# Kernel tuning notes

Measured on AMD Instinct MI355X. Metric: run time of the kernel, lower is better.

The kernel has to match this reference:

```python
import jax, jax.numpy as jnp
import numpy as np

B, N, D, H = 4, 4096, 512, 8
K = D // H  # per-head dim = 64


def setup_inputs() -> dict:
    key = jax.random.key(0)
    k1, k2, k3, k4 = jax.random.split(key, 4)
    x = jax.random.normal(k1, (B, N, D), dtype=jnp.float32)
    # Conv1d(D, K, 1, bias=False) -> weight matrix [K, D], kaiming fan_out
    Wa = jax.random.normal(k2, (K, D), dtype=jnp.float32) * np.float32(np.sqrt(2.0 / K))
    # Conv1d(K, 1, 1) -> weight vector [K], bias scalar (init 0.01)
    Wb = jax.random.normal(k3, (K,), dtype=jnp.float32) * np.float32(np.sqrt(2.0))
    Wc = jax.random.normal(k4, (K,), dtype=jnp.float32) * np.float32(np.sqrt(2.0))
    wb_bias = jnp.full((), 0.01, dtype=jnp.float32)
    wc_bias = jnp.full((), 0.01, dtype=jnp.float32)
    bias = jnp.full((K,), 0.01, dtype=jnp.float32)
    return {"batchinput": x, "Wa": Wa, "Wb": Wb, "wb_bias": wb_bias,
            "Wc": Wc, "wc_bias": wc_bias, "bias": bias}


def reference(batchinput, Wa, Wb, wb_bias, Wc, wc_bias, bias):
    # single step (n_steps=1); all n_head heads share weights, so mean over
    # identical heads equals one head (dropout=0.0 -> identity).
    h = jnp.einsum('bnd,kd->bnk', batchinput, Wa)            # [B,N,K] projected feats
    t1 = jnp.einsum('bnk,k->bn', h, Wb) + wb_bias            # [B,N]
    t2 = jnp.einsum('bnk,k->bn', h, Wc) + wc_bias            # [B,N]
    scores = t1[:, :, None] + t2[:, None, :]                 # [B,N,N] additive score
    coefs = jax.nn.softmax(jax.nn.leaky_relu(scores, negative_slope=0.2), axis=-1)
    out = jnp.einsum('bnm,bmk->bnk', coefs, h) + bias        # [B,N,K]
    return out
```

## Files before the change

kernel.cpp:

```cpp
#include <hip/hip_runtime.h>
#include <hip/hip_bf16.h>

constexpr int cB = 4;
constexpr int cN = 4096;
constexpr int cD = 512;
constexpr int cK = 64;
constexpr int cNB = cB * cN;
constexpr int cNP = cN + 1;
constexpr int cCS = 16;
constexpr int cNC = cN / cCS;
constexpr int cNC1 = cNC + 1;

typedef unsigned short u16;
typedef unsigned int u32;
typedef unsigned long long u64;
typedef __bf16 bf16x8 __attribute__((ext_vector_type(8)));
typedef float f32x4 __attribute__((ext_vector_type(4)));

constexpr size_t OFF_H    = 0;
constexpr size_t OFF_T1   = OFF_H    + (size_t)cNB * cK;
constexpr size_t OFF_T2   = OFF_T1   + cNB;
constexpr size_t OFF_T2S  = OFF_T2   + cNB;
constexpr size_t OFF_IDX  = OFF_T2S  + cNB;
constexpr size_t OFF_P    = OFF_IDX  + cNB;
constexpr size_t OFF_EPL  = OFF_P    + cNB;
constexpr size_t OFF_GNL  = OFF_EPL  + (size_t)cB * cNP * cK;
constexpr size_t OFF_EPS  = OFF_GNL  + (size_t)cB * cNP * cK;
constexpr size_t OFF_GNS  = OFF_EPS  + (size_t)cB * cNP;
constexpr size_t OFF_CHE  = OFF_GNS  + (size_t)cB * cNP;
constexpr size_t OFF_CHG  = OFF_CHE  + (size_t)cB * cNC * cK;
constexpr size_t OFF_CHES = OFF_CHG  + (size_t)cB * cNC * cK;
constexpr size_t OFF_CHGS = OFF_CHES + (size_t)cB * cNC;
constexpr size_t OFF_OFE  = OFF_CHGS + (size_t)cB * cNC;
constexpr size_t OFF_OFG  = OFF_OFE  + (size_t)cB * cNC1 * cK;
constexpr size_t OFF_OFES = OFF_OFG  + (size_t)cB * cNC1 * cK;
constexpr size_t OFF_OFGS = OFF_OFES + (size_t)cB * cNC1;
constexpr size_t OFF_XB16 = OFF_OFGS + (size_t)cB * cNC1;
constexpr size_t OFF_WB16 = OFF_XB16 + (size_t)cNB * cD / 2;

__device__ __forceinline__ u16 f2bf(float f) {
    unsigned u = __float_as_uint(f);
    u += 0x7fffu + ((u >> 16) & 1u);
    return (u16)(u >> 16);
}
__device__ __forceinline__ u32 pk2(float a, float b) {
    return (u32)f2bf(a) | ((u32)f2bf(b) << 16);
}
__device__ __forceinline__ u32 f2sort(float f) {
    u32 b = __float_as_uint(f);
    u32 mask = (u32)((int)b >> 31);
    return b ^ (mask | 0x80000000u);
}

__global__ __launch_bounds__(256) void k_prep(
    const float* __restrict__ x, const float* __restrict__ Wa,
    const float* __restrict__ Wb, const float* __restrict__ wbb,
    const float* __restrict__ Wc, const float* __restrict__ wcb,
    u16* __restrict__ xb16, u16* __restrict__ wab16,
    float* __restrict__ t1, float* __restrict__ t2)
{
    __shared__ float wabL[cD], wacL[cD];
    int t = threadIdx.x;
    if (blockIdx.x >= 512) {
        int i4 = (((int)blockIdx.x - 512) * 256 + t) * 4;
        float4 v = *(const float4*)(Wa + i4);
        uint2 p = {pk2(v.x, v.y), pk2(v.z, v.w)};
        *(uint2*)(wab16 + i4) = p;
        return;
    }
    float s1a = 0.f, s2a = 0.f, s1b = 0.f, s2b = 0.f;
#pragma unroll 8
    for (int k = 0; k < cK; ++k) {
        float wbk = Wb[k], wck = Wc[k];
        float wa1 = Wa[k * cD + t];
        float wa2 = Wa[k * cD + t + 256];
        s1a += wa1 * wbk; s2a += wa1 * wck;
        s1b += wa2 * wbk; s2b += wa2 * wck;
    }
    wabL[t] = s1a; wacL[t] = s2a; wabL[t + 256] = s1b; wacL[t + 256] = s2b;
    __syncthreads();

    int w = t >> 6, lane = t & 63;
    int d1 = lane * 4, d2 = 256 + lane * 4;
    float4 wbA = *(const float4*)&wabL[d1], wbB = *(const float4*)&wabL[d2];
    float4 wcA = *(const float4*)&wacL[d1], wcB = *(const float4*)&wacL[d2];
    float wbbv = wbb[0], wcbv = wcb[0];
#pragma unroll 2
    for (int rr = 0; rr < 8; ++rr) {
        int row = blockIdx.x * 32 + w * 8 + rr;
        const float* xp = x + (size_t)row * cD;
        float4 a  = *(const float4*)(xp + d1);
        float4 bq = *(const float4*)(xp + d2);
        uint2 pa = {pk2(a.x, a.y), pk2(a.z, a.w)};
        uint2 pb = {pk2(bq.x, bq.y), pk2(bq.z, bq.w)};
        *(uint2*)(xb16 + (size_t)row * cD + d1) = pa;
        *(uint2*)(xb16 + (size_t)row * cD + d2) = pb;
        float p1 = a.x*wbA.x + a.y*wbA.y + a.z*wbA.z + a.w*wbA.w
                 + bq.x*wbB.x + bq.y*wbB.y + bq.z*wbB.z + bq.w*wbB.w;
        float p2 = a.x*wcA.x + a.y*wcA.y + a.z*wcA.z + a.w*wcA.w
                 + bq.x*wcB.x + bq.y*wcB.y + bq.z*wcB.z + bq.w*wcB.w;
#pragma unroll
        for (int off = 32; off > 0; off >>= 1) {
            p1 += __shfl_down(p1, off, 64);
            p2 += __shfl_down(p2, off, 64);
        }
        if (lane == 0) { t1[row] = p1 + wbbv; t2[row] = p2 + wcbv; }
    }
}

__global__ __launch_bounds__(256) void k_projrank(
    const u16* __restrict__ xb16, const u16* __restrict__ wab16,
    const float* __restrict__ t1, const float* __restrict__ t2,
    float* __restrict__ h, float* __restrict__ t2s, int* __restrict__ idxs,
    int* __restrict__ pidx)
{
    __shared__ __align__(16) u64 shbuf[4096 + 256];
    int t = threadIdx.x;
    if (blockIdx.x < 256) {
        u16* xs = (u16*)shbuf;
        u16* was = xs + 64 * 32;
        int rowbase = blockIdx.x * 64;
        int w = t >> 6, lane = t & 63, m = lane & 15, quad = lane >> 4;
        int grow = w * 16 + (lane >> 2);
        int gcol = (lane & 3) * 8;
        const u16* xg = xb16 + (size_t)(rowbase + grow) * cD + gcol;
        const u16* wg = wab16 + (size_t)grow * cD + gcol;
        int lidx = grow * 32 + gcol;

        f32x4 acc[4] = {{0.f,0.f,0.f,0.f},{0.f,0.f,0.f,0.f},
                        {0.f,0.f,0.f,0.f},{0.f,0.f,0.f,0.f}};
        uint4 xv = *(const uint4*)(xg);
        uint4 wv = *(const uint4*)(wg);
        for (int s = 0; s < 16; ++s) {
            __syncthreads();
            *(uint4*)&xs[lidx] = xv;
            *(uint4*)&was[lidx] = wv;
            if (s < 15) {
                xv = *(const uint4*)(xg + (s + 1) * 32);
                wv = *(const uint4*)(wg + (s + 1) * 32);
            }
            __syncthreads();
            bf16x8 av = *(const bf16x8*)&xs[(w * 16 + m) * 32 + quad * 8];
#pragma unroll
            for (int g = 0; g < 4; ++g) {
                bf16x8 bv = *(const bf16x8*)&was[(g * 16 + m) * 32 + quad * 8];
                acc[g] = __builtin_amdgcn_mfma_f32_16x16x32_bf16(av, bv, acc[g], 0, 0, 0);
            }
        }
#pragma unroll
        for (int g = 0; g < 4; ++g) {
#pragma unroll
            for (int r4 = 0; r4 < 4; ++r4) {
                int row = w * 16 + quad * 4 + r4;
                h[(size_t)(rowbase + row) * cK + g * 16 + m] = acc[g][r4];
            }
        }
    } else {
        u64* keys = shbuf;
        int* part = (int*)(shbuf + 4096);
        int rb = blockIdx.x - 256;
        int b = rb >> 6;
        int rowgrp = rb & 63;
        for (int i = t; i < cN; i += 256)
            keys[i] = ((u64)f2sort(t2[b * cN + i]) << 32) | (u32)i;
        __syncthreads();
        int lane = t & 63, subset = t >> 6;
        int myrow = rowgrp * 64 + lane;
        u64 mykey = keys[myrow];
        u32 pk_hi = f2sort(-t1[(size_t)b * cN + myrow]);
        int s0 = subset * 1024;
        int cnt = 0, cnt2 = 0;
#pragma unroll 8
        for (int kk = 0; kk < 1024; ++kk) {
            u64 kv = keys[s0 + kk];
            cnt  += (kv < mykey) ? 1 : 0;
            cnt2 += ((u32)(kv >> 32) < pk_hi) ? 1 : 0;
        }
        part[subset * 64 + lane] = cnt;
        part[256 + subset * 64 + lane] = cnt2;
        __syncthreads();
        if (t < 64) {
            int jj = rowgrp * 64 + t;
            int rank = part[t] + part[64 + t] + part[128 + t] + part[192 + t];
            int pc   = part[256 + t] + part[320 + t] + part[384 + t] + part[448 + t];
            t2s[b * cN + rank] = t2[b * cN + jj];
            idxs[b * cN + rank] = jj;
            pidx[b * cN + jj] = pc;
        }
    }
}

__global__ __launch_bounds__(64) void k_chunkscan(
    const float* __restrict__ t2s, const int* __restrict__ idxs,
    const float* __restrict__ h,
    float* __restrict__ EpL, float* __restrict__ GnL,
    float* __restrict__ eps_l, float* __restrict__ gns_l,
    float* __restrict__ chE, float* __restrict__ chG,
    float* __restrict__ chEs, float* __restrict__ chGs)
{
    int lane = threadIdx.x;
    int blk = blockIdx.x;
    int c = blk & (cNC - 1);
    int b = blk >> 8;
    int base = b * cN + c * cCS;
    size_t rowbase = ((size_t)b * cNP + c * cCS) * cK;
    int sbase = b * cNP + c * cCS;
    float M2 = t2s[b * cN + cN - 1];
    int   idxv = (lane < cCS) ? idxs[base + lane] : 0;
    float t2v  = (lane < cCS) ? t2s[base + lane] : 0.f;

    float hv[cCS];
#pragma unroll
    for (int i = 0; i < cCS; ++i) {
        int j = __shfl(idxv, i, 64);
        hv[i] = h[((size_t)b * cN + j) * cK + lane];
    }
    float ee[cCS], gg[cCS];
#pragma unroll
    for (int i = 0; i < cCS; ++i) {
        float d = __shfl(t2v, i, 64) - M2;
        ee[i] = __expf(d);
        gg[i] = __expf(0.2f * d);
    }
    if (c == cNC - 1) {
        EpL[((size_t)b * cNP + cN) * cK + lane] = 0.f;
        GnL[((size_t)b * cNP + cN) * cK + lane] = 0.f;
        if (lane == 0) { eps_l[b * cNP + cN] = 0.f; gns_l[b * cNP + cN] = 0.f; }
    }
    float acc = 0.f, accs = 0.f;
#pragma unroll
    for (int i = cCS - 1; i >= 0; --i) {
        acc += ee[i] * hv[i]; accs += ee[i];
        EpL[rowbase + (size_t)i * cK + lane] = acc;
        if (lane == 0) eps_l[sbase + i] = accs;
    }
    chE[((size_t)b * cNC + c) * cK + lane] = acc;
    if (lane == 0) chEs[b * cNC + c] = accs;
    acc = 0.f; accs = 0.f;
#pragma unroll
    for (int i = 0; i < cCS; ++i) {
        GnL[rowbase + (size_t)i * cK + lane] = acc;
        if (lane == 0) gns_l[sbase + i] = accs;
        acc += gg[i] * hv[i]; accs += gg[i];
    }
    chG[((size_t)b * cNC + c) * cK + lane] = acc;
    if (lane == 0) chGs[b * cNC + c] = accs;
}

__global__ __launch_bounds__(1024) void k_offsets(
    const float* __restrict__ chE, const float* __restrict__ chG,
    const float* __restrict__ chEs, const float* __restrict__ chGs,
    float* __restrict__ ofE, float* __restrict__ ofG,
    float* __restrict__ ofEs, float* __restrict__ ofGs)
{
    __shared__ float wsum[16][64];
    int t = threadIdx.x;
    int lane = t & 63, w = t >> 6;
    int dir = blockIdx.x & 1;
    int b = blockIdx.x >> 1;
    const float* ch = dir ? chG : chE;
    float* of = dir ? ofG : ofE;
    int c0 = w * 16;

    float cv[16];
    float s = 0.f;
#pragma unroll
    for (int i = 0; i < 16; ++i) {
        cv[i] = ch[((size_t)b * cNC + c0 + i) * cK + lane];
        s += cv[i];
    }
    wsum[w][lane] = s;
    __syncthreads();
    float base = 0.f;
    if (dir == 0) { for (int w2 = w + 1; w2 < 16; ++w2) base += wsum[w2][lane]; }
    else          { for (int w2 = 0; w2 < w; ++w2) base += wsum[w2][lane]; }

    if (dir == 0) {
        float run = base;
#pragma unroll
        for (int i = 15; i >= 0; --i) {
            of[((size_t)b * cNC1 + c0 + i) * cK + lane] = run;
            run += cv[i];
        }
        if (w == 0) of[((size_t)b * cNC1 + cNC) * cK + lane] = 0.f;
    } else {
        float run = base;
#pragma unroll
        for (int i = 0; i < 16; ++i) {
            of[((size_t)b * cNC1 + c0 + i) * cK + lane] = run;
            run += cv[i];
        }
        if (w == 15) of[((size_t)b * cNC1 + cNC) * cK + lane] = run;
    }

    if (w == 0) {
        const float* chs = dir ? chGs : chEs;
        float* ofs = dir ? ofGs : ofEs;
        float e0 = chs[b * cNC + lane * 4 + 0];
        float e1 = chs[b * cNC + lane * 4 + 1];
        float e2 = chs[b * cNC + lane * 4 + 2];
        float e3 = chs[b * cNC + lane * 4 + 3];
        float p = e0 + e1 + e2 + e3;
        if (dir == 0) {
            float s2 = p;
#pragma unroll
            for (int off = 1; off < 64; off <<= 1) {
                float tv = __shfl_down(s2, off, 64);
                if (lane + off < 64) s2 += tv;
            }
            float excl = s2 - p;
            ofs[b * cNC1 + lane * 4 + 0] = excl + e1 + e2 + e3;
            ofs[b * cNC1 + lane * 4 + 1] = excl + e2 + e3;
            ofs[b * cNC1 + lane * 4 + 2] = excl + e3;
            ofs[b * cNC1 + lane * 4 + 3] = excl;
            if (lane == 0) ofs[b * cNC1 + cNC] = 0.f;
        } else {
            float s2 = p;
#pragma unroll
            for (int off = 1; off < 64; off <<= 1) {
                float tv = __shfl_up(s2, off, 64);
                if (lane >= off) s2 += tv;
            }
            float excl = s2 - p;
            ofs[b * cNC1 + lane * 4 + 0] = excl;
            ofs[b * cNC1 + lane * 4 + 1] = excl + e0;
            ofs[b * cNC1 + lane * 4 + 2] = excl + e0 + e1;
            ofs[b * cNC1 + lane * 4 + 3] = excl + e0 + e1 + e2;
            if (lane == 63) ofs[b * cNC1 + cNC] = s2;
        }
    }
}

__global__ __launch_bounds__(256) void k_out(
    const float* __restrict__ t1, const float* __restrict__ t2s,
    const int* __restrict__ pidx,
    const float* __restrict__ EpL, const float* __restrict__ GnL,
    const float* __restrict__ eps_l, const float* __restrict__ gns_l,
    const float* __restrict__ ofE, const float* __restrict__ ofG,
    const float* __restrict__ ofEs, const float* __restrict__ ofGs,
    const float* __restrict__ bias, float* __restrict__ out)
{
    int tid = threadIdx.x;
    int lane = tid & 63;
    int r = blockIdx.x * 4 + (tid >> 6);
    int b = r >> 12;
    float T1 = t1[r];
    float M2 = t2s[b * cN + cN - 1];
    float smax = T1 + M2;
    float m = fmaxf(smax, 0.2f * smax);
    float A  = __expf(smax - m);
    float Cc = __expf(0.2f * smax - m);
    int p = pidx[r];
    int c = p >> 4;
    size_t pr = ((size_t)b * cNP + p) * cK + lane;
    size_t cr = ((size_t)b * cNC1 + c) * cK + lane;
    float num = A * (EpL[pr] + ofE[cr]) + Cc * (GnL[pr] + ofG[cr]);
    float den = A * (eps_l[(size_t)b * cNP + p] + ofEs[b * cNC1 + c])
              + Cc * (gns_l[(size_t)b * cNP + p] + ofGs[b * cNC1 + c]);
    out[(size_t)r * cK + lane] = num / den + bias[lane];
}

extern "C" void kernel_launch(void* const* d_in, const int* in_sizes, int n_in,
                              void* d_out, int out_size, void* d_ws, size_t ws_size,
                              hipStream_t stream)
{
    const float* x    = (const float*)d_in[0];
    const float* Wa   = (const float*)d_in[1];
    const float* Wb   = (const float*)d_in[2];
    const float* wbb  = (const float*)d_in[3];
    const float* Wc   = (const float*)d_in[4];
    const float* wcb  = (const float*)d_in[5];
    const float* bias = (const float*)d_in[6];
    float* out = (float*)d_out;

    float* ws = (float*)d_ws;
    float* h     = ws + OFF_H;
    float* t1    = ws + OFF_T1;
    float* t2    = ws + OFF_T2;
    float* t2s   = ws + OFF_T2S;
    int*   idxs  = (int*)(ws + OFF_IDX);
    int*   pidx  = (int*)(ws + OFF_P);
    float* EpL   = ws + OFF_EPL;
    float* GnL   = ws + OFF_GNL;
    float* eps_l = ws + OFF_EPS;
    float* gns_l = ws + OFF_GNS;
    float* chE   = ws + OFF_CHE;
    float* chG   = ws + OFF_CHG;
    float* chEs  = ws + OFF_CHES;
    float* chGs  = ws + OFF_CHGS;
    float* ofE   = ws + OFF_OFE;
    float* ofG   = ws + OFF_OFG;
    float* ofEs  = ws + OFF_OFES;
    float* ofGs  = ws + OFF_OFGS;
    u16*   xb16  = (u16*)(ws + OFF_XB16);
    u16*   wab16 = (u16*)(ws + OFF_WB16);

    k_prep<<<544, 256, 0, stream>>>(x, Wa, Wb, wbb, Wc, wcb, xb16, wab16, t1, t2);
    k_projrank<<<512, 256, 0, stream>>>(xb16, wab16, t1, t2, h, t2s, idxs, pidx);
    k_chunkscan<<<cB * cNC, 64, 0, stream>>>(t2s, idxs, h, EpL, GnL, eps_l, gns_l,
                                             chE, chG, chEs, chGs);
    k_offsets<<<cB * 2, 1024, 0, stream>>>(chE, chG, chEs, chGs, ofE, ofG, ofEs, ofGs);
    k_out<<<cNB / 4, 256, 0, stream>>>(t1, t2s, pidx, EpL, GnL, eps_l, gns_l,
                                       ofE, ofG, ofEs, ofGs, bias, out);
}
```

Measured before the change: 130.4 us.

## Fuse five-kernel pipeline into one cooperative persistent kernel with grid syncs

Replaces the five separate launches (prep, projection+rank, chunk scan, offsets, output) with a single cooperative kernel of 256 blocks of 512 threads. Phases are separated by grid.sync(). Each block keeps its bf16-converted x tile in swizzled shared memory and reuses it for the MFMA projection, so the bf16 copy of x no longer round-trips through global memory. This removes the gaps between kernel launches, at the cost of grid-wide barriers, lower occupancy (one block per CU) and phases where most blocks sit idle, such as the offset scan that uses only 8 blocks. It falls back to the old launches if the cooperative launch fails.

```diff
diff --git a/kernel.cpp b/kernel.cpp
--- a/kernel.cpp
+++ b/kernel.cpp
@@ -1,5 +1,8 @@
 #include <hip/hip_runtime.h>
 #include <hip/hip_bf16.h>
+#include <hip/hip_cooperative_groups.h>
+
+namespace cg = cooperative_groups;
 
 constexpr int cB = 4;
 constexpr int cN = 4096;
@@ -52,6 +55,299 @@
     return b ^ (mask | 0x80000000u);
 }
 
+__global__ __launch_bounds__(512, 1) void k_mega(
+    const float* __restrict__ x, const float* __restrict__ Wa,
+    const float* __restrict__ Wb, const float* __restrict__ wbb,
+    const float* __restrict__ Wc, const float* __restrict__ wcb,
+    const float* __restrict__ bias, float* __restrict__ out,
+    float* __restrict__ t1, float* __restrict__ t2,
+    float* __restrict__ t2s, int* __restrict__ idxs, int* __restrict__ pidx,
+    u16* __restrict__ wab16, float* __restrict__ h,
+    float* __restrict__ EpL, float* __restrict__ GnL,
+    float* __restrict__ eps_l, float* __restrict__ gns_l,
+    float* __restrict__ chE, float* __restrict__ chG,
+    float* __restrict__ chEs, float* __restrict__ chGs,
+    float* __restrict__ ofE, float* __restrict__ ofG,
+    float* __restrict__ ofEs, float* __restrict__ ofGs)
+{
+    extern __shared__ char smem[];
+    cg::grid_group grid = cg::this_grid();
+    int t = threadIdx.x;
+    int blk = blockIdx.x;
+    float* wabL = (float*)(smem + 65536);
+    float* wacL = wabL + cD;
+
+    {
+        float s1 = 0.f, s2 = 0.f;
+#pragma unroll 8
+        for (int k = 0; k < cK; ++k) {
+            float w = Wa[k * cD + t];
+            s1 += w * Wb[k];
+            s2 += w * Wc[k];
+        }
+        wabL[t] = s1; wacL[t] = s2;
+        if (blk < 16) {
+            int i4 = (blk * 512 + t) * 4;
+            float4 v = *(const float4*)(Wa + i4);
+            uint2 p = {pk2(v.x, v.y), pk2(v.z, v.w)};
+            *(uint2*)(wab16 + i4) = p;
+        }
+    }
+    __syncthreads();
+
+    {
+        int row = t >> 3, s8 = t & 7;
+        int rowg = blk * 64 + row;
+        const float* xr = x + (size_t)rowg * cD;
+        float p1 = 0.f, p2 = 0.f;
+        char* arow = smem + row * 1024;
+        unsigned swz = (unsigned)(row & 7) << 4;
+#pragma unroll
+        for (int i = 0; i < 8; ++i) {
+            int col = i * 64 + s8 * 8;
+            float4 a  = *(const float4*)(xr + col);
+            float4 b  = *(const float4*)(xr + col + 4);
+            float4 wa1 = *(const float4*)(wabL + col);
+            float4 wa2 = *(const float4*)(wabL + col + 4);
+            float4 wc1 = *(const float4*)(wacL + col);
+            float4 wc2 = *(const float4*)(wacL + col + 4);
+            p1 += a.x*wa1.x + a.y*wa1.y + a.z*wa1.z + a.w*wa1.w
+                + b.x*wa2.x + b.y*wa2.y + b.z*wa2.z + b.w*wa2.w;
+            p2 += a.x*wc1.x + a.y*wc1.y + a.z*wc1.z + a.w*wc1.w
+                + b.x*wc2.x + b.y*wc2.y + b.z*wc2.z + b.w*wc2.w;
+            uint4 pk = {pk2(a.x, a.y), pk2(a.z, a.w), pk2(b.x, b.y), pk2(b.z, b.w)};
+            *(uint4*)(arow + (((unsigned)(col * 2)) ^ swz)) = pk;
+        }
+        p1 += __shfl_xor(p1, 1, 64); p1 += __shfl_xor(p1, 2, 64); p1 += __shfl_xor(p1, 4, 64);
+        p2 += __shfl_xor(p2, 1, 64); p2 += __shfl_xor(p2, 2, 64); p2 += __shfl_xor(p2, 4, 64);
+        if (s8 == 0) { t1[rowg] = p1 + wbb[0]; t2[rowg] = p2 + wcb[0]; }
+    }
+    __threadfence();
+    grid.sync();
+
+    {
+        u64* keys = (u64*)(smem + 65536);
+        int* part = (int*)(smem + 98304);
+        int b = blk >> 6, rowgrp = blk & 63;
+        const float* t2b = t2 + (size_t)b * cN;
+        for (int i = t; i < cN; i += 512)
+            keys[i] = ((u64)f2sort(t2b[i]) << 32) | (u32)i;
+        __syncthreads();
+        int lane = t & 63, subset = t >> 6;
+        int myrow = rowgrp * 64 + lane;
+        u64 mykey = keys[myrow];
+        u32 pk_hi = f2sort(-t1[(size_t)b * cN + myrow]);
+        int s0 = subset * 512;
+        int cnt = 0, cnt2 = 0;
+#pragma unroll 8
+        for (int kk = 0; kk < 512; ++kk) {
+            u64 kv = keys[s0 + kk];
+            cnt  += (kv < mykey) ? 1 : 0;
+            cnt2 += ((u32)(kv >> 32) < pk_hi) ? 1 : 0;
+        }
+        part[subset * 64 + lane] = cnt;
+        part[512 + subset * 64 + lane] = cnt2;
+        __syncthreads();
+        if (t < 64) {
+            int jj = rowgrp * 64 + t;
+            int rank = 0, pc = 0;
+#pragma unroll
+            for (int s = 0; s < 8; ++s) {
+                rank += part[s * 64 + t];
+                pc   += part[512 + s * 64 + t];
+            }
+            t2s[(size_t)b * cN + rank] = t2b[jj];
+            idxs[(size_t)b * cN + rank] = jj;
+            pidx[(size_t)b * cN + jj] = pc;
+        }
+    }
+
+    {
+        int w = t >> 6, lane = t & 63, m = lane & 15, quad = lane >> 4;
+        int rowblk = (w & 3) * 16;
+        int g0 = (w >> 2) * 2;
+        f32x4 acc0 = {0.f, 0.f, 0.f, 0.f}, acc1 = {0.f, 0.f, 0.f, 0.f};
+        int arow_ = rowblk + m;
+        const char* abase = smem + arow_ * 1024;
+        unsigned swz = (unsigned)(arow_ & 7) << 4;
+        const u16* bg0 = wab16 + (size_t)(g0 * 16 + m) * cD + quad * 8;
+        const u16* bg1 = wab16 + (size_t)((g0 + 1) * 16 + m) * cD + quad * 8;
+#pragma unroll 4
+        for (int s = 0; s < 16; ++s) {
+            bf16x8 av  = *(const bf16x8*)(abase + (((unsigned)(s * 64 + quad * 16)) ^ swz));
+            bf16x8 bv0 = *(const bf16x8*)(bg0 + s * 32);
+            bf16x8 bv1 = *(const bf16x8*)(bg1 + s * 32);
+            acc0 = __builtin_amdgcn_mfma_f32_16x16x32_bf16(av, bv0, acc0, 0, 0, 0);
+            acc1 = __builtin_amdgcn_mfma_f32_16x16x32_bf16(av, bv1, acc1, 0, 0, 0);
+        }
+        int rowbase = blk * 64;
+#pragma unroll
+        for (int r4 = 0; r4 < 4; ++r4) {
+            int row = rowblk + quad * 4 + r4;
+            h[(size_t)(rowbase + row) * cK + g0 * 16 + m]       = acc0[r4];
+            h[(size_t)(rowbase + row) * cK + (g0 + 1) * 16 + m] = acc1[r4];
+        }
+    }
+    __threadfence();
+    grid.sync();
+
+    {
+        int w = t >> 6, lane = t & 63;
+        int unit = blk * 4 + (w & 3);
+        int role = w >> 2;
+        int b = unit >> 8, c = unit & (cNC - 1);
+        int base = b * cN + c * cCS;
+        size_t rowbase = ((size_t)b * cNP + c * cCS) * cK;
+        int sbase = b * cNP + c * cCS;
+        float M2 = t2s[(size_t)b * cN + cN - 1];
+        int   idxv = (lane < cCS) ? idxs[base + lane] : 0;
+        float t2v  = (lane < cCS) ? t2s[base + lane] : 0.f;
+        float hv[cCS];
+#pragma unroll
+        for (int i = 0; i < cCS; ++i) {
+            int j = __shfl(idxv, i, 64);
+            hv[i] = h[((size_t)b * cN + j) * cK + lane];
+        }
+        float slope = role ? 0.2f : 1.0f;
+        float ev[cCS];
+#pragma unroll
+        for (int i = 0; i < cCS; ++i)
+            ev[i] = __expf(slope * (__shfl(t2v, i, 64) - M2));
+        if (role == 0) {
+            if (c == cNC - 1) {
+                EpL[((size_t)b * cNP + cN) * cK + lane] = 0.f;
+                if (lane == 0) eps_l[b * cNP + cN] = 0.f;
+            }
+            float acc = 0.f, accs = 0.f;
+#pragma unroll
+            for (int i = cCS - 1; i >= 0; --i) {
+                acc += ev[i] * hv[i]; accs += ev[i];
+                EpL[rowbase + (size_t)i * cK + lane] = acc;
+                if (lane == 0) eps_l[sbase + i] = accs;
+            }
+            chE[((size_t)b * cNC + c) * cK + lane] = acc;
+            if (lane == 0) chEs[b * cNC + c] = accs;
+        } else {
+            if (c == cNC - 1) {
+                GnL[((size_t)b * cNP + cN) * cK + lane] = 0.f;
+                if (lane == 0) gns_l[b * cNP + cN] = 0.f;
+            }
+            float acc = 0.f, accs = 0.f;
+#pragma unroll
+            for (int i = 0; i < cCS; ++i) {
+                GnL[rowbase + (size_t)i * cK + lane] = acc;
+                if (lane == 0) gns_l[sbase + i] = accs;
+                acc += ev[i] * hv[i]; accs += ev[i];
+            }
+            chG[((size_t)b * cNC + c) * cK + lane] = acc;
+            if (lane == 0) chGs[b * cNC + c] = accs;
+        }
+    }
+    __threadfence();
+    grid.sync();
+
+    if (blk < 8) {
+        float (*wsum)[64] = (float(*)[64])(smem + 98304);
+        int lane = t & 63, w = t >> 6;
+        int dir = blk & 1;
+        int b = blk >> 1;
+        const float* ch = dir ? chG : chE;
+        float* of = dir ? ofG : ofE;
+        int c0 = w * 32;
+        float cv[32];
+        float s = 0.f;
+#pragma unroll
+        for (int i = 0; i < 32; ++i) {
+            cv[i] = ch[((size_t)b * cNC + c0 + i) * cK + lane];
+            s += cv[i];
+        }
+        wsum[w][lane] = s;
+        __syncthreads();
+        float base = 0.f;
+        if (dir == 0) { for (int w2 = w + 1; w2 < 8; ++w2) base += wsum[w2][lane]; }
+        else          { for (int w2 = 0; w2 < w; ++w2) base += wsum[w2][lane]; }
+        if (dir == 0) {
+            float run = base;
+#pragma unroll
+            for (int i = 31; i >= 0; --i) {
+                of[((size_t)b * cNC1 + c0 + i) * cK + lane] = run;
+                run += cv[i];
+            }
+            if (w == 0) of[((size_t)b * cNC1 + cNC) * cK + lane] = 0.f;
+        } else {
+            float run = base;
+#pragma unroll
+            for (int i = 0; i < 32; ++i) {
+                of[((size_t)b * cNC1 + c0 + i) * cK + lane] = run;
+                run += cv[i];
+            }
+            if (w == 7) of[((size_t)b * cNC1 + cNC) * cK + lane] = run;
+        }
+        if (w == 0) {
+            const float* chs = dir ? chGs : chEs;
+            float* ofs = dir ? ofGs : ofEs;
+            float e0 = chs[b * cNC + lane * 4 + 0];
+            float e1 = chs[b * cNC + lane * 4 + 1];
+            float e2 = chs[b * cNC + lane * 4 + 2];
+            float e3 = chs[b * cNC + lane * 4 + 3];
+            float p = e0 + e1 + e2 + e3;
+            if (dir == 0) {
+                float s2 = p;
+#pragma unroll
+                for (int off = 1; off < 64; off <<= 1) {
+                    float tv = __shfl_down(s2, off, 64);
+                    if (lane + off < 64) s2 += tv;
+                }
+                float excl = s2 - p;
+                ofs[b * cNC1 + lane * 4 + 0] = excl + e1 + e2 + e3;
+                ofs[b * cNC1 + lane * 4 + 1] = excl + e2 + e3;
+                ofs[b * cNC1 + lane * 4 + 2] = excl + e3;
+                ofs[b * cNC1 + lane * 4 + 3] = excl;
+                if (lane == 0) ofs[b * cNC1 + cNC] = 0.f;
+            } else {
+                float s2 = p;
+#pragma unroll
+                for (int off = 1; off < 64; off <<= 1) {
+                    float tv = __shfl_up(s2, off, 64);
+                    if (lane >= off) s2 += tv;
+                }
+                float excl = s2 - p;
+                ofs[b * cNC1 + lane * 4 + 0] = excl;
+                ofs[b * cNC1 + lane * 4 + 1] = excl + e0;
+                ofs[b * cNC1 + lane * 4 + 2] = excl + e0 + e1;
+                ofs[b * cNC1 + lane * 4 + 3] = excl + e0 + e1 + e2;
+                if (lane == 63) ofs[b * cNC1 + cNC] = s2;
+            }
+        }
+    }
+    __threadfence();
+    grid.sync();
+
+    {
+        int w = t >> 6, lane = t & 63;
+        float bv = bias[lane];
+#pragma unroll
+        for (int i = 0; i < 8; ++i) {
+            int r = blk * 64 + w * 8 + i;
+            int b = r >> 12;
+            float T1 = t1[r];
+            float M2 = t2s[(size_t)b * cN + cN - 1];
+            float smax = T1 + M2;
+            float m = fmaxf(smax, 0.2f * smax);
+            float A  = __expf(smax - m);
+            float Cc = __expf(0.2f * smax - m);
+            int p = pidx[r];
+            int c = p >> 4;
+            size_t pr = ((size_t)b * cNP + p) * cK + lane;
+            size_t cr = ((size_t)b * cNC1 + c) * cK + lane;
+            float num = A * (EpL[pr] + ofE[cr]) + Cc * (GnL[pr] + ofG[cr]);
+            float den = A * (eps_l[(size_t)b * cNP + p] + ofEs[b * cNC1 + c])
+                      + Cc * (gns_l[(size_t)b * cNP + p] + ofGs[b * cNC1 + c]);
+            out[(size_t)r * cK + lane] = num / den + bv;
+        }
+    }
+}
+
 __global__ __launch_bounds__(256) void k_prep(
     const float* __restrict__ x, const float* __restrict__ Wa,
     const float* __restrict__ Wb, const float* __restrict__ wbb,
@@ -143,8 +439,8 @@
             bf16x8 av = *(const bf16x8*)&xs[(w * 16 + m) * 32 + quad * 8];
 #pragma unroll
             for (int g = 0; g < 4; ++g) {
-                bf16x8 bv = *(const bf16x8*)&was[(g * 16 + m) * 32 + quad * 8];
-                acc[g] = __builtin_amdgcn_mfma_f32_16x16x32_bf16(av, bv, acc[g], 0, 0, 0);
+                bf16x8 bvv = *(const bf16x8*)&was[(g * 16 + m) * 32 + quad * 8];
+                acc[g] = __builtin_amdgcn_mfma_f32_16x16x32_bf16(av, bvv, acc[g], 0, 0, 0);
             }
         }
 #pragma unroll
@@ -395,6 +691,27 @@
     u16*   xb16  = (u16*)(ws + OFF_XB16);
     u16*   wab16 = (u16*)(ws + OFF_WB16);
 
+    constexpr unsigned SMEM = 102400;
+    static int use_coop = -1;
+    if (use_coop < 0) {
+        hipError_t e = hipFuncSetAttribute((const void*)k_mega,
+            hipFuncAttributeMaxDynamicSharedMemorySize, (int)SMEM);
+        use_coop = (e == hipSuccess) ? 1 : 0;
+    }
+    if (use_coop) {
+        void* args[] = {
+            (void*)&x, (void*)&Wa, (void*)&Wb, (void*)&wbb, (void*)&Wc, (void*)&wcb,
+            (void*)&bias, (void*)&out, (void*)&t1, (void*)&t2, (void*)&t2s,
+            (void*)&idxs, (void*)&pidx, (void*)&wab16, (void*)&h,
+            (void*)&EpL, (void*)&GnL, (void*)&eps_l, (void*)&gns_l,
+            (void*)&chE, (void*)&chG, (void*)&chEs, (void*)&chGs,
+            (void*)&ofE, (void*)&ofG, (void*)&ofEs, (void*)&ofGs };
+        hipError_t e = hipLaunchCooperativeKernel((const void*)k_mega,
+            dim3(256), dim3(512), args, SMEM, stream);
+        if (e == hipSuccess) return;
+        use_coop = 0;
+    }
+
     k_prep<<<544, 256, 0, stream>>>(x, Wa, Wb, wbb, Wc, wcb, xb16, wab16, t1, t2);
     k_projrank<<<512, 256, 0, stream>>>(xb16, wab16, t1, t2, h, t2s, idxs, pidx);
     k_chunkscan<<<cB * cNC, 64, 0, stream>>>(t2s, idxs, h, EpL, GnL, eps_l, gns_l,
```

After: 413.9 us. 3.17x slower.

## Fuse bf16 conversion into projection, split chunkscan roles, fuse offsets into output

Applied to the files above, without the earlier changes.

Stops writing a bf16 copy of x in the prep kernel. The projection kernel now reads fp32 x and converts it while staging into LDS, which saves a full write and re-read of the activations. The chunk scan now launches separate blocks for the E and G directions so each block does half the exponentials and stores. The offsets kernel is fused into a new output kernel: each block recomputes the per-batch chunk prefix sums in a large LDS buffer (about 131 KB) and then produces outputs. This removes one launch and the global offset arrays, at the cost of redundant prefix-sum work across 64 blocks per batch and occupancy limited to one block per CU.

```diff
diff --git a/kernel.cpp b/kernel.cpp
--- a/kernel.cpp
+++ b/kernel.cpp
@@ -35,8 +35,7 @@
 constexpr size_t OFF_OFG  = OFF_OFE  + (size_t)cB * cNC1 * cK;
 constexpr size_t OFF_OFES = OFF_OFG  + (size_t)cB * cNC1 * cK;
 constexpr size_t OFF_OFGS = OFF_OFES + (size_t)cB * cNC1;
-constexpr size_t OFF_XB16 = OFF_OFGS + (size_t)cB * cNC1;
-constexpr size_t OFF_WB16 = OFF_XB16 + (size_t)cNB * cD / 2;
+constexpr size_t OFF_WB16 = OFF_OFGS + (size_t)cB * cNC1;
 
 __device__ __forceinline__ u16 f2bf(float f) {
     unsigned u = __float_as_uint(f);
@@ -56,8 +55,7 @@
     const float* __restrict__ x, const float* __restrict__ Wa,
     const float* __restrict__ Wb, const float* __restrict__ wbb,
     const float* __restrict__ Wc, const float* __restrict__ wcb,
-    u16* __restrict__ xb16, u16* __restrict__ wab16,
-    float* __restrict__ t1, float* __restrict__ t2)
+    u16* __restrict__ wab16, float* __restrict__ t1, float* __restrict__ t2)
 {
     __shared__ float wabL[cD], wacL[cD];
     int t = threadIdx.x;
@@ -91,10 +89,6 @@
         const float* xp = x + (size_t)row * cD;
         float4 a  = *(const float4*)(xp + d1);
         float4 bq = *(const float4*)(xp + d2);
-        uint2 pa = {pk2(a.x, a.y), pk2(a.z, a.w)};
-        uint2 pb = {pk2(bq.x, bq.y), pk2(bq.z, bq.w)};
-        *(uint2*)(xb16 + (size_t)row * cD + d1) = pa;
-        *(uint2*)(xb16 + (size_t)row * cD + d2) = pb;
         float p1 = a.x*wbA.x + a.y*wbA.y + a.z*wbA.z + a.w*wbA.w
                  + bq.x*wbB.x + bq.y*wbB.y + bq.z*wbB.z + bq.w*wbB.w;
         float p2 = a.x*wcA.x + a.y*wcA.y + a.z*wcA.z + a.w*wcA.w
@@ -109,7 +103,7 @@
 }
 
 __global__ __launch_bounds__(256) void k_projrank(
-    const u16* __restrict__ xb16, const u16* __restrict__ wab16,
+    const float* __restrict__ x, const u16* __restrict__ wab16,
     const float* __restrict__ t1, const float* __restrict__ t2,
     float* __restrict__ h, float* __restrict__ t2s, int* __restrict__ idxs,
     int* __restrict__ pidx)
@@ -123,28 +117,32 @@
         int w = t >> 6, lane = t & 63, m = lane & 15, quad = lane >> 4;
         int grow = w * 16 + (lane >> 2);
         int gcol = (lane & 3) * 8;
-        const u16* xg = xb16 + (size_t)(rowbase + grow) * cD + gcol;
+        const float* xg = x + (size_t)(rowbase + grow) * cD + gcol;
         const u16* wg = wab16 + (size_t)grow * cD + gcol;
         int lidx = grow * 32 + gcol;
 
         f32x4 acc[4] = {{0.f,0.f,0.f,0.f},{0.f,0.f,0.f,0.f},
                         {0.f,0.f,0.f,0.f},{0.f,0.f,0.f,0.f}};
-        uint4 xv = *(const uint4*)(xg);
+        float4 xa = *(const float4*)(xg);
+        float4 xb2 = *(const float4*)(xg + 4);
         uint4 wv = *(const uint4*)(wg);
         for (int s = 0; s < 16; ++s) {
             __syncthreads();
+            uint4 xv = {pk2(xa.x, xa.y), pk2(xa.z, xa.w),
+                        pk2(xb2.x, xb2.y), pk2(xb2.z, xb2.w)};
             *(uint4*)&xs[lidx] = xv;
             *(uint4*)&was[lidx] = wv;
             if (s < 15) {
-                xv = *(const uint4*)(xg + (s + 1) * 32);
+                xa  = *(const float4*)(xg + (s + 1) * 32);
+                xb2 = *(const float4*)(xg + (s + 1) * 32 + 4);
                 wv = *(const uint4*)(wg + (s + 1) * 32);
             }
             __syncthreads();
             bf16x8 av = *(const bf16x8*)&xs[(w * 16 + m) * 32 + quad * 8];
 #pragma unroll
             for (int g = 0; g < 4; ++g) {
-                bf16x8 bv = *(const bf16x8*)&was[(g * 16 + m) * 32 + quad * 8];
-                acc[g] = __builtin_amdgcn_mfma_f32_16x16x32_bf16(av, bv, acc[g], 0, 0, 0);
+                bf16x8 bvv = *(const bf16x8*)&was[(g * 16 + m) * 32 + quad * 8];
+                acc[g] = __builtin_amdgcn_mfma_f32_16x16x32_bf16(av, bvv, acc[g], 0, 0, 0);
             }
         }
 #pragma unroll
@@ -199,9 +197,10 @@
     float* __restrict__ chEs, float* __restrict__ chGs)
 {
     int lane = threadIdx.x;
-    int blk = blockIdx.x;
-    int c = blk & (cNC - 1);
-    int b = blk >> 8;
+    int role = blockIdx.x & 1;
+    int unit = blockIdx.x >> 1;
+    int c = unit & (cNC - 1);
+    int b = unit >> 8;
     int base = b * cN + c * cCS;
     size_t rowbase = ((size_t)b * cNP + c * cCS) * cK;
     int sbase = b * cNP + c * cCS;
@@ -215,36 +214,147 @@
         int j = __shfl(idxv, i, 64);
         hv[i] = h[((size_t)b * cN + j) * cK + lane];
     }
-    float ee[cCS], gg[cCS];
-#pragma unroll
-    for (int i = 0; i < cCS; ++i) {
-        float d = __shfl(t2v, i, 64) - M2;
-        ee[i] = __expf(d);
-        gg[i] = __expf(0.2f * d);
-    }
-    if (c == cNC - 1) {
-        EpL[((size_t)b * cNP + cN) * cK + lane] = 0.f;
-        GnL[((size_t)b * cNP + cN) * cK + lane] = 0.f;
-        if (lane == 0) { eps_l[b * cNP + cN] = 0.f; gns_l[b * cNP + cN] = 0.f; }
-    }
-    float acc = 0.f, accs = 0.f;
-#pragma unroll
-    for (int i = cCS - 1; i >= 0; --i) {
-        acc += ee[i] * hv[i]; accs += ee[i];
-        EpL[rowbase + (size_t)i * cK + lane] = acc;
-        if (lane == 0) eps_l[sbase + i] = accs;
-    }
-    chE[((size_t)b * cNC + c) * cK + lane] = acc;
-    if (lane == 0) chEs[b * cNC + c] = accs;
-    acc = 0.f; accs = 0.f;
-#pragma unroll
-    for (int i = 0; i < cCS; ++i) {
-        GnL[rowbase + (size_t)i * cK + lane] = acc;
-        if (lane == 0) gns_l[sbase + i] = accs;
-        acc += gg[i] * hv[i]; accs += gg[i];
-    }
-    chG[((size_t)b * cNC + c) * cK + lane] = acc;
-    if (lane == 0) chGs[b * cNC + c] = accs;
+    float slope = role ? 0.2f : 1.0f;
+    float ev[cCS];
+#pragma unroll
+    for (int i = 0; i < cCS; ++i)
+        ev[i] = __expf(slope * (__shfl(t2v, i, 64) - M2));
+
+    if (role == 0) {
+        if (c == cNC - 1) {
+            EpL[((size_t)b * cNP + cN) * cK + lane] = 0.f;
+            if (lane == 0) eps_l[b * cNP + cN] = 0.f;
+        }
+        float acc = 0.f, accs = 0.f;
+#pragma unroll
+        for (int i = cCS - 1; i >= 0; --i) {
+            acc += ev[i] * hv[i]; accs += ev[i];
+            EpL[rowbase + (size_t)i * cK + lane] = acc;
+            if (lane == 0) eps_l[sbase + i] = accs;
+        }
+        chE[((size_t)b * cNC + c) * cK + lane] = acc;
+        if (lane == 0) chEs[b * cNC + c] = accs;
+    } else {
+        if (c == cNC - 1) {
+            GnL[((size_t)b * cNP + cN) * cK + lane] = 0.f;
+            if (lane == 0) gns_l[b * cNP + cN] = 0.f;
+        }
+        float acc = 0.f, accs = 0.f;
+#pragma unroll
+        for (int i = 0; i < cCS; ++i) {
+            GnL[rowbase + (size_t)i * cK + lane] = acc;
+            if (lane == 0) gns_l[sbase + i] = accs;
+            acc += ev[i] * hv[i]; accs += ev[i];
+        }
+        chG[((size_t)b * cNC + c) * cK + lane] = acc;
+        if (lane == 0) chGs[b * cNC + c] = accs;
+    }
+}
+
+constexpr unsigned SMEM_OUT = 134664;
+__global__ __launch_bounds__(256, 1) void k_outf(
+    const float* __restrict__ t1, const float* __restrict__ t2s,
+    const int* __restrict__ pidx,
+    const float* __restrict__ EpL, const float* __restrict__ GnL,
+    const float* __restrict__ eps_l, const float* __restrict__ gns_l,
+    const float* __restrict__ chE, const float* __restrict__ chG,
+    const float* __restrict__ chEs, const float* __restrict__ chGs,
+    const float* __restrict__ bias, float* __restrict__ out)
+{
+    extern __shared__ char sm[];
+    float (*ofEl)[64] = (float(*)[64])(sm);
+    float (*ofGl)[64] = (float(*)[64])(sm + 65792);
+    float* ofEsL      = (float*)(sm + 131584);
+    float* ofGsL      = (float*)(sm + 132612);
+    float (*wsum)[64] = (float(*)[64])(sm + 133640);
+
+    int t = threadIdx.x, lane = t & 63, w = t >> 6;
+    int blk = blockIdx.x;
+    int b = blk >> 6;
+    const float* chEb = chE + (size_t)b * cNC * cK;
+    const float* chGb = chG + (size_t)b * cNC * cK;
+    int c0 = w * 64;
+
+    {
+        float cv[64]; float s = 0.f;
+#pragma unroll
+        for (int i = 0; i < 64; ++i) { cv[i] = chEb[(size_t)(c0 + i) * cK + lane]; s += cv[i]; }
+        wsum[w][lane] = s;
+        if (w == 0) {
+            float e0 = chEs[b*cNC + lane*4+0], e1 = chEs[b*cNC + lane*4+1];
+            float e2 = chEs[b*cNC + lane*4+2], e3 = chEs[b*cNC + lane*4+3];
+            float p = e0+e1+e2+e3, s2 = p;
+#pragma unroll
+            for (int off = 1; off < 64; off <<= 1) {
+                float tv = __shfl_down(s2, off, 64);
+                if (lane + off < 64) s2 += tv;
+            }
+            float excl = s2 - p;
+            ofEsL[lane*4+0] = excl + e1 + e2 + e3;
+            ofEsL[lane*4+1] = excl + e2 + e3;
+            ofEsL[lane*4+2] = excl + e3;
+            ofEsL[lane*4+3] = excl;
+            if (lane == 0) ofEsL[cNC] = 0.f;
+        } else if (w == 1) {
+            float e0 = chGs[b*cNC + lane*4+0], e1 = chGs[b*cNC + lane*4+1];
+            float e2 = chGs[b*cNC + lane*4+2], e3 = chGs[b*cNC + lane*4+3];
+            float p = e0+e1+e2+e3, s2 = p;
+#pragma unroll
+            for (int off = 1; off < 64; off <<= 1) {
+                float tv = __shfl_up(s2, off, 64);
+                if (lane >= off) s2 += tv;
+            }
+            float excl = s2 - p;
+            ofGsL[lane*4+0] = excl;
+            ofGsL[lane*4+1] = excl + e0;
+            ofGsL[lane*4+2] = excl + e0 + e1;
+            ofGsL[lane*4+3] = excl + e0 + e1 + e2;
+            if (lane == 63) ofGsL[cNC] = s2;
+        }
+        __syncthreads();
+        float base = 0.f;
+        for (int w2 = w + 1; w2 < 4; ++w2) base += wsum[w2][lane];
+        float run = base;
+#pragma unroll
+        for (int i = 63; i >= 0; --i) { ofEl[c0 + i][lane] = run; run += cv[i]; }
+        if (w == 0) ofEl[cNC][lane] = 0.f;
+    }
+    __syncthreads();
+    {
+        float cv[64]; float s = 0.f;
+#pragma unroll
+        for (int i = 0; i < 64; ++i) { cv[i] = chGb[(size_t)(c0 + i) * cK + lane]; s += cv[i]; }
+        wsum[w][lane] = s;
+        __syncthreads();
+        float base = 0.f;
+        for (int w2 = 0; w2 < w; ++w2) base += wsum[w2][lane];
+        float run = base;
+#pragma unroll
+        for (int i = 0; i < 64; ++i) { ofGl[c0 + i][lane] = run; run += cv[i]; }
+        if (w == 3) ofGl[cNC][lane] = run;
+    }
+    __syncthreads();
+
+    float bv = bias[lane];
+    float M2 = t2s[(size_t)b * cN + cN - 1];
+    int r0 = blk * 64 + w * 16;
+    const float* epsb = eps_l + (size_t)b * cNP;
+    const float* gnsb = gns_l + (size_t)b * cNP;
+#pragma unroll 8
+    for (int i = 0; i < 16; ++i) {
+        int r = r0 + i;
+        float T1 = t1[r];
+        float smax = T1 + M2;
+        float m = fmaxf(smax, 0.2f * smax);
+        float A  = __expf(smax - m);
+        float Cc = __expf(0.2f * smax - m);
+        int p = pidx[r];
+        int c = p >> 4;
+        size_t pr = ((size_t)b * cNP + p) * cK + lane;
+        float num = A * (EpL[pr] + ofEl[c][lane]) + Cc * (GnL[pr] + ofGl[c][lane]);
+        float den = A * (epsb[p] + ofEsL[c]) + Cc * (gnsb[p] + ofGsL[c]);
+        out[(size_t)r * cK + lane] = num / den + bv;
+    }
 }
 
 __global__ __launch_bounds__(1024) void k_offsets(
@@ -392,14 +502,25 @@
     float* ofG   = ws + OFF_OFG;
     float* ofEs  = ws + OFF_OFES;
     float* ofGs  = ws + OFF_OFGS;
-    u16*   xb16  = (u16*)(ws + OFF_XB16);
     u16*   wab16 = (u16*)(ws + OFF_WB16);
 
-    k_prep<<<544, 256, 0, stream>>>(x, Wa, Wb, wbb, Wc, wcb, xb16, wab16, t1, t2);
-    k_projrank<<<512, 256, 0, stream>>>(xb16, wab16, t1, t2, h, t2s, idxs, pidx);
-    k_chunkscan<<<cB * cNC, 64, 0, stream>>>(t2s, idxs, h, EpL, GnL, eps_l, gns_l,
-                                             chE, chG, chEs, chGs);
-    k_offsets<<<cB * 2, 1024, 0, stream>>>(chE, chG, chEs, chGs, ofE, ofG, ofEs, ofGs);
-    k_out<<<cNB / 4, 256, 0, stream>>>(t1, t2s, pidx, EpL, GnL, eps_l, gns_l,
-                                       ofE, ofG, ofEs, ofGs, bias, out);
-}
+    static int use_big_lds = -1;
+    if (use_big_lds < 0) {
+        hipError_t e = hipFuncSetAttribute((const void*)k_outf,
+            hipFuncAttributeMaxDynamicSharedMemorySize, (int)SMEM_OUT);
+        use_big_lds = (e == hipSuccess) ? 1 : 0;
+    }
+
+    k_prep<<<544, 256, 0, stream>>>(x, Wa, Wb, wbb, Wc, wcb, wab16, t1, t2);
+    k_projrank<<<512, 256, 0, stream>>>(x, wab16, t1, t2, h, t2s, idxs, pidx);
+    k_chunkscan<<<cB * cNC * 2, 64, 0, stream>>>(t2s, idxs, h, EpL, GnL, eps_l, gns_l,
+                                                 chE, chG, chEs, chGs);
+    if (use_big_lds) {
+        k_outf<<<256, 256, SMEM_OUT, stream>>>(t1, t2s, pidx, EpL, GnL, eps_l, gns_l,
+                                               chE, chG, chEs, chGs, bias, out);
+    } else {
+        k_offsets<<<cB * 2, 1024, 0, stream>>>(chE, chG, chEs, chGs, ofE, ofG, ofEs, ofGs);
+        k_out<<<cNB / 4, 256, 0, stream>>>(t1, t2s, pidx, EpL, GnL, eps_l, gns_l,
+                                           ofE, ofG, ofEs, ofGs, bias, out);
+    }
+}
```

Result: faster. 126.7 us (-2.8%).
